# Kernel optimization log

Measured on AMD Instinct MI355X. Metric: run time of the kernel, lower is better.

## Reference

```python
import jax, jax.numpy as jnp
import numpy as np

NUM_USERS = 30000
NUM_ITEMS = 70000
N = NUM_USERS + NUM_ITEMS
D = 128
NNZ = 1_000_000
N_LAYERS = 3
BATCH = 16384
EPS = 1e-12  # torch F.normalize default eps
SLOPE = 0.01  # nn.LeakyReLU default negative_slope


def setup_inputs() -> dict:
    key = jax.random.key(0)
    ks = jax.random.split(key, 12)
    return {
        "userIdx": jax.random.randint(ks[0], (BATCH,), 0, NUM_USERS),
        "itemIdx": jax.random.randint(ks[1], (BATCH,), 0, NUM_ITEMS),
        "rows": jax.random.randint(ks[2], (NNZ,), 0, N),
        "cols": jax.random.randint(ks[3], (NNZ,), 0, N),
        "vals": jax.random.uniform(ks[4], (NNZ,), dtype=jnp.float32) * 0.1,
        "uEmbd": jax.random.normal(ks[5], (NUM_USERS, D), dtype=jnp.float32) * 0.1,
        "iEmbd": jax.random.normal(ks[6], (NUM_ITEMS, D), dtype=jnp.float32) * 0.1,
        "Wlin": jax.random.normal(ks[7], (N_LAYERS, D, D), dtype=jnp.float32) / np.sqrt(D),
        "blin": jax.random.normal(ks[8], (N_LAYERS, D), dtype=jnp.float32) * 0.01,
        "Wint": jax.random.normal(ks[9], (N_LAYERS, D, D), dtype=jnp.float32) / np.sqrt(D),
        "bint": jax.random.normal(ks[10], (N_LAYERS, D), dtype=jnp.float32) * 0.01,
    }


def reference(userIdx, itemIdx, rows, cols, vals, uEmbd, iEmbd, Wlin, blin, Wint, bint):
    num_users = uEmbd.shape[0]
    n = uEmbd.shape[0] + iEmbd.shape[0]
    features = jnp.concatenate([uEmbd, iEmbd], axis=0)  # [N, D]
    embds = [features]
    for l in range(Wlin.shape[0]):
        # SpMM: L @ features via gather + segment_sum over COO edges
        Lx = jax.ops.segment_sum(vals[:, None] * features[cols], rows, num_segments=n)
        # (L + I) @ f then linear
        part1 = (Lx + features) @ Wlin[l] + blin[l]
        # (L @ f) * f then linear
        part2 = (Lx * features) @ Wint[l] + bint[l]
        features = jax.nn.leaky_relu(part1 + part2, negative_slope=SLOPE)
        norm = jnp.maximum(jnp.linalg.norm(features, axis=1, keepdims=True), EPS)
        features = features / norm
        embds.append(features)
    finalEmbd = jnp.concatenate(embds, axis=1)  # [N, D*(1+n_layers)]
    u = finalEmbd[userIdx]
    i = finalEmbd[itemIdx + num_users]
    return jnp.sum(u * i, axis=1)
```

## Files before the change

kernel.cpp:

```cpp
#include <hip/hip_runtime.h>
#include <hip/hip_bf16.h>

#define NU 30000
#define NI 70000
#define NN 100000
#define DD 128
#define NLAYERS 3
#define SLOPE_ 0.01f
#define EPS_ 1e-12f

#define NB 782
#define NBKT 1024
#define NBLK 256
#define AROW 136
#define MAXL 32768
#define BM 64

typedef __bf16 v8bf __attribute__((ext_vector_type(8)));
typedef float v16f __attribute__((ext_vector_type(16)));
typedef float v2f __attribute__((ext_vector_type(2)));
typedef unsigned short ushort_t;

union UB8 { uint4 u; v8bf v; };

__device__ __forceinline__ float bflo(unsigned u) { return __uint_as_float(u << 16); }
__device__ __forceinline__ float bfhi(unsigned u) { return __uint_as_float(u & 0xffff0000u); }

__device__ __forceinline__ unsigned pk2(float a, float b) {
    __hip_bfloat162 h = __float22bfloat162_rn(make_float2(a, b));
    return *reinterpret_cast<unsigned*>(&h);
}
__device__ __forceinline__ uint4 pk8(const float* f) {
    return make_uint4(pk2(f[0], f[1]), pk2(f[2], f[3]), pk2(f[4], f[5]), pk2(f[6], f[7]));
}
__device__ __forceinline__ void unp8(uint4 g, float* f) {
    f[0] = bflo(g.x); f[1] = bfhi(g.x);
    f[2] = bflo(g.y); f[3] = bfhi(g.y);
    f[4] = bflo(g.z); f[5] = bfhi(g.z);
    f[6] = bflo(g.w); f[7] = bfhi(g.w);
}
__device__ __forceinline__ ushort_t f2bf1(float x) {
    __hip_bfloat16 h = __float2bfloat16(x);
    return *reinterpret_cast<ushort_t*>(&h);
}

__global__ __launch_bounds__(256) void k_concat_bf(const float* __restrict__ u,
                                                   const float* __restrict__ it,
                                                   ushort_t* __restrict__ fb) {
    int idx = blockIdx.x * 256 + threadIdx.x;
    if (idx >= NN * DD / 8) return;
    size_t base = (size_t)idx * 8;
    const float* src = (base < (size_t)NU * DD) ? (u + base) : (it + base - (size_t)NU * DD);
    float f[8];
    float4 a = *(const float4*)src;
    float4 b = *(const float4*)(src + 4);
    f[0] = a.x; f[1] = a.y; f[2] = a.z; f[3] = a.w;
    f[4] = b.x; f[5] = b.y; f[6] = b.z; f[7] = b.w;
    *(uint4*)(fb + base) = pk8(f);
}

__device__ __forceinline__ void dot_body(const ushort_t* __restrict__ fb,
                                         const int* __restrict__ uIdx,
                                         const int* __restrict__ iIdx,
                                         float* __restrict__ out,
                                         int batch, int accum, int blk, int t) {
    int b = blk * 4 + (t >> 6);
    if (b >= batch) return;
    int lane = t & 63;
    unsigned ua = *(const unsigned*)(fb + (size_t)uIdx[b] * DD + lane * 2);
    unsigned ib = *(const unsigned*)(fb + (size_t)(iIdx[b] + NU) * DD + lane * 2);
    float s = bflo(ua) * bflo(ib) + bfhi(ua) * bfhi(ib);
#pragma unroll
    for (int m = 32; m; m >>= 1) s += __shfl_xor(s, m, 64);
    if (lane == 0) out[b] = accum ? out[b] + s : s;
}

__global__ __launch_bounds__(256) void k_dot(const ushort_t* __restrict__ fb,
                                             const int* __restrict__ uIdx,
                                             const int* __restrict__ iIdx,
                                             float* __restrict__ out,
                                             int batch, int accum) {
    dot_body(fb, uIdx, iIdx, out, batch, accum, blockIdx.x, threadIdx.x);
}

__global__ __launch_bounds__(256) void k_lhist(const int* __restrict__ rows,
                                               int* __restrict__ ghist,
                                               int* __restrict__ flags,
                                               int nnz, int epb) {
    __shared__ int h[NBKT];
    int t = threadIdx.x, b = blockIdx.x;
#pragma unroll
    for (int i = 0; i < 4; ++i) h[t + 256 * i] = 0;
    for (int i = b * 256 + t; i < NN; i += NBLK * 256) flags[i] = 0;
    __syncthreads();
    int e0 = b * epb, e1 = min(e0 + epb, nnz);
    for (int e = e0 + t; e < e1; e += 256) atomicAdd(&h[rows[e] >> 7], 1);
    __syncthreads();
#pragma unroll
    for (int i = 0; i < 4; ++i) {
        int bkt = t + 256 * i;
        ghist[bkt * NBLK + b] = h[bkt];
    }
}

__global__ __launch_bounds__(256) void k_rscan(int* __restrict__ ghist,
                                               int* __restrict__ btot,
                                               const int* __restrict__ uIdx,
                                               const int* __restrict__ iIdx,
                                               int* __restrict__ flags,
                                               int* __restrict__ cnt, int batch) {
    int t = threadIdx.x;
    int gid = blockIdx.x * 256 + t;
    if (gid == 0) *cnt = 0;
    if (gid < batch) flags[uIdx[gid]] = 1;
    else if (gid < 2 * batch) flags[iIdx[gid - batch] + NU] = 1;

    int bkt = blockIdx.x * 4 + (t >> 6);
    int lane = t & 63;
    int* row = ghist + bkt * NBLK;
    int4 c = *(const int4*)(row + lane * 4);
    int s = c.x + c.y + c.z + c.w;
    int incl = s;
#pragma unroll
    for (int m = 1; m < 64; m <<= 1) {
        int o = __shfl_up(incl, m, 64);
        if (lane >= m) incl += o;
    }
    int excl = incl - s;
    int4 o;
    o.x = excl;
    o.y = o.x + c.x;
    o.z = o.y + c.y;
    o.w = o.z + c.z;
    *(int4*)(row + lane * 4) = o;
    if (lane == 63) btot[bkt] = incl;
}

__global__ __launch_bounds__(256) void k_btscan(const int* __restrict__ btot,
                                                int* __restrict__ bbase) {
    int t = threadIdx.x;
    int4 c = *(const int4*)(btot + t * 4);
    int tsum = c.x + c.y + c.z + c.w;
    int incl = tsum;
#pragma unroll
    for (int m = 1; m < 64; m <<= 1) {
        int o = __shfl_up(incl, m, 64);
        if ((t & 63) >= m) incl += o;
    }
    __shared__ int wsum[4];
    if ((t & 63) == 63) wsum[t >> 6] = incl;
    __syncthreads();
    int off = 0;
    for (int i = 0; i < (t >> 6); ++i) off += wsum[i];
    int excl = off + incl - tsum;
    int4 o;
    o.x = excl;
    o.y = o.x + c.x;
    o.z = o.y + c.y;
    o.w = o.z + c.z;
    *(int4*)(bbase + t * 4) = o;
    if (t == 255) bbase[NBKT] = o.w + c.w;
}

__global__ __launch_bounds__(256) void k_sscatter(const int* __restrict__ rows,
                                                  const int* __restrict__ cols,
                                                  const float* __restrict__ vals,
                                                  const int* __restrict__ ghist,
                                                  const int* __restrict__ bbase,
                                                  int2* __restrict__ bedges,
                                                  const int* __restrict__ flags,
                                                  int* __restrict__ list,
                                                  int* __restrict__ cnt,
                                                  int nnz, int epb) {
    __shared__ int base[NBKT];
    __shared__ int h[NBKT];
    int t = threadIdx.x, b = blockIdx.x;
#pragma unroll
    for (int i = 0; i < 4; ++i) {
        int bkt = t + 256 * i;
        base[bkt] = bbase[bkt] + ghist[bkt * NBLK + b];
        h[bkt] = 0;
    }
    int lane = t & 63;
    for (int i = b * 256 + t; i < ((NN + 65535) & ~65535); i += NBLK * 256) {
        int f = (i < NN) ? flags[i] : 0;
        unsigned long long mask = __ballot(f);
        int total = __popcll(mask);
        int prefix = __popcll(mask & ((1ULL << lane) - 1));
        int bs = 0;
        if (lane == 0 && total) bs = atomicAdd(cnt, total);
        bs = __shfl(bs, 0, 64);
        if (f) list[bs + prefix] = i;
    }
    __syncthreads();
    int e0 = b * epb, e1 = min(e0 + epb, nnz);
    for (int e = e0 + t; e < e1; e += 256) {
        int r = rows[e];
        int bkt = r >> 7;
        int rank = atomicAdd(&h[bkt], 1);
        bedges[base[bkt] + rank] = make_int2(((r & 127) << 20) | cols[e],
                                             __float_as_int(vals[e]));
    }
}

__global__ __launch_bounds__(256) void k_csort(const int* __restrict__ bbase,
                                               const int2* __restrict__ bedges,
                                               int2* __restrict__ edges,
                                               int* __restrict__ rowPtr, int nnz) {
    __shared__ int cntS[128];
    __shared__ int fillS[128];
    __shared__ int wtot;
    int b = blockIdx.x, t = threadIdx.x;
    int s0 = bbase[b];
    int s1 = bbase[b + 1];
    if (t < 128) cntS[t] = 0;
    __syncthreads();
    for (int i = s0 + t; i < s1; i += 256) atomicAdd(&cntS[bedges[i].x >> 20], 1);
    __syncthreads();
    int v = 0, incl = 0;
    if (t < 128) {
        v = cntS[t];
        incl = v;
#pragma unroll
        for (int m = 1; m < 64; m <<= 1) {
            int o = __shfl_up(incl, m, 64);
            if ((t & 63) >= m) incl += o;
        }
        if (t == 63) wtot = incl;
    }
    __syncthreads();
    if (t < 128) {
        int excl = incl - v + ((t >= 64) ? wtot : 0);
        fillS[t] = excl;
        int gr = b * 128 + t;
        if (gr < NN) rowPtr[gr] = s0 + excl;
    }
    if (b == 0 && t == 0) rowPtr[NN] = nnz;
    __syncthreads();
    for (int i = s0 + t; i < s1; i += 256) {
        int2 e = bedges[i];
        int r = e.x >> 20;
        int p = atomicAdd(&fillS[r], 1);
        edges[s0 + p] = make_int2(e.x & 0xFFFFF, e.y);
    }
}

__global__ __launch_bounds__(256) void k_wprep(const float* __restrict__ Wlin,
                                               const float* __restrict__ Wint,
                                               uint4* __restrict__ Wb4) {
    int id = blockIdx.x * 256 + threadIdx.x;
    int lane = id & 63;
    int w = (id >> 6) & 3;
    int s = (id >> 8) & 7;
    int c = (id >> 11) & 1;
    int l = id >> 12;
    const float* src = (c ? Wint : Wlin) + (size_t)l * DD * DD;
    int n = w * 32 + (lane & 31);
    int k0 = s * 16 + ((lane >> 5) & 1) * 8;
    float f[8];
#pragma unroll
    for (int j = 0; j < 8; ++j) f[j] = src[(size_t)(k0 + j) * DD + n];
    Wb4[id] = pk8(f);
}

__device__ __forceinline__ void acc_pk(v2f* acc2, uint4 g, float v) {
    v2f vv = {v, v};
    unsigned gw[4] = {g.x, g.y, g.z, g.w};
#pragma unroll
    for (int p = 0; p < 4; ++p) {
        v2f x = {bflo(gw[p]), bfhi(gw[p])};
        acc2[p] = x * vv + acc2[p];
    }
}

__device__ __forceinline__ void spmm_row(int r, int l,
                                         const int* __restrict__ rowPtr,
                                         const int2* __restrict__ edges,
                                         const ushort_t* __restrict__ fb,
                                         ushort_t* __restrict__ Lxb) {
    int q = l >> 4;
    int d0 = (l & 15) * 8;
    int beg = rowPtr[r], end = rowPtr[r + 1];
    v2f acc2[4];
#pragma unroll
    for (int p = 0; p < 4; ++p) acc2[p] = (v2f){0.f, 0.f};
    int e = beg + q;
    for (; e + 4 < end; e += 8) {
        int2 p0 = edges[e];
        int2 p1 = edges[e + 4];
        uint4 g0 = *(const uint4*)(fb + (size_t)p0.x * DD + d0);
        uint4 g1 = *(const uint4*)(fb + (size_t)p1.x * DD + d0);
        acc_pk(acc2, g0, __int_as_float(p0.y));
        acc_pk(acc2, g1, __int_as_float(p1.y));
    }
    if (e < end) {
        int2 p0 = edges[e];
        uint4 g0 = *(const uint4*)(fb + (size_t)p0.x * DD + d0);
        acc_pk(acc2, g0, __int_as_float(p0.y));
    }
    float acc[8];
#pragma unroll
    for (int p = 0; p < 4; ++p) { acc[2 * p] = acc2[p][0]; acc[2 * p + 1] = acc2[p][1]; }
#pragma unroll
    for (int j = 0; j < 8; ++j) {
        acc[j] += __shfl_xor(acc[j], 16, 64);
        acc[j] += __shfl_xor(acc[j], 32, 64);
    }
    if (l < 16) *(uint4*)(Lxb + (size_t)r * DD + d0) = pk8(acc);
}

__global__ __launch_bounds__(256) void k_spmm_dot(const int* __restrict__ rowPtr,
                                                  const int2* __restrict__ edges,
                                                  const ushort_t* __restrict__ fb,
                                                  ushort_t* __restrict__ Lxb,
                                                  const int* __restrict__ uIdx,
                                                  const int* __restrict__ iIdx,
                                                  float* __restrict__ out,
                                                  int batch, int accum, int dotBlocks) {
    if ((int)blockIdx.x < dotBlocks) {
        dot_body(fb, uIdx, iIdx, out, batch, accum, blockIdx.x, threadIdx.x);
        return;
    }
    int r = (blockIdx.x - dotBlocks) * 4 + (threadIdx.x >> 6);
    if (r >= NN) return;
    spmm_row(r, threadIdx.x & 63, rowPtr, edges, fb, Lxb);
}

__global__ __launch_bounds__(256) void k_spmm_idx_dot(const int* __restrict__ rowPtr,
                                                      const int2* __restrict__ edges,
                                                      const ushort_t* __restrict__ fb,
                                                      ushort_t* __restrict__ Lxb,
                                                      const int* __restrict__ list,
                                                      const int* __restrict__ cnt,
                                                      const int* __restrict__ uIdx,
                                                      const int* __restrict__ iIdx,
                                                      float* __restrict__ out,
                                                      int batch, int dotBlocks) {
    if ((int)blockIdx.x < dotBlocks) {
        dot_body(fb, uIdx, iIdx, out, batch, 1, blockIdx.x, threadIdx.x);
        return;
    }
    int i = (blockIdx.x - dotBlocks) * 4 + (threadIdx.x >> 6);
    if (i >= *cnt) return;
    spmm_row(list[i], threadIdx.x & 63, rowPtr, edges, fb, Lxb);
}

template <bool INDEXED>
__device__ __forceinline__ void layer_body(const ushort_t* __restrict__ Lxb,
                                           const uint4* __restrict__ Wb4,
                                           const float* __restrict__ blin,
                                           const float* __restrict__ bint,
                                           ushort_t* __restrict__ fb,
                                           const ushort_t* __restrict__ fin,
                                           const int* __restrict__ list, int nc) {
    __shared__ ushort_t As[BM * AROW];
    __shared__ float pnormAll[BM * 4];
    __shared__ float rinvS[BM];
    __shared__ int rowIdS[BM];

    const int t = threadIdx.x;
    const int w = t >> 6;
    const int l = t & 63;
    const int q = l >> 5;
    const int ln = l & 31;
    const int n = w * 32 + ln;
    const int m0 = blockIdx.x * BM;

    if (INDEXED && m0 >= nc) return;

    if (t < BM) {
        int gi = m0 + t;
        int gm;
        if (INDEXED) gm = (gi < nc) ? list[gi] : -1;
        else gm = (gi < NN) ? gi : -1;
        rowIdS[t] = gm;
    }
    __syncthreads();

    const float bias = blin[n] + bint[n];

    v16f acc[2];
#pragma unroll
    for (int mt = 0; mt < 2; ++mt)
#pragma unroll
        for (int i = 0; i < 16; ++i) acc[mt][i] = 0.f;

    for (int c = 0; c < 2; ++c) {
#pragma unroll
        for (int ii = 0; ii < 4; ++ii) {
            int idx = ii * 256 + t;
            int row = idx >> 4;
            int ch = idx & 15;
            int gm = rowIdS[row];
            uint4 outv = make_uint4(0, 0, 0, 0);
            if (gm >= 0) {
                uint4 gl = *(const uint4*)(Lxb + (size_t)gm * DD + ch * 8);
                uint4 gf = *(const uint4*)(fin + (size_t)gm * DD + ch * 8);
                float a[8], b[8], r[8];
                unp8(gl, a);
                unp8(gf, b);
                if (c == 0) {
#pragma unroll
                    for (int j = 0; j < 8; ++j) r[j] = a[j] + b[j];
                } else {
#pragma unroll
                    for (int j = 0; j < 8; ++j) r[j] = a[j] * b[j];
                }
                outv = pk8(r);
            }
            *(uint4*)&As[row * AROW + ch * 8] = outv;
        }
        __syncthreads();

        UB8 bf[8];
#pragma unroll
        for (int s = 0; s < 8; ++s) bf[s].u = Wb4[c * 2048 + s * 256 + w * 64 + l];

#pragma unroll
        for (int mt = 0; mt < 2; ++mt) {
#pragma unroll
            for (int s = 0; s < 8; ++s) {
                v8bf af = *(const v8bf*)&As[(mt * 32 + ln) * AROW + s * 16 + q * 8];
                acc[mt] = __builtin_amdgcn_mfma_f32_32x32x16_bf16(af, bf[s].v, acc[mt], 0, 0, 0);
            }
        }
        __syncthreads();
    }

#pragma unroll
    for (int mt = 0; mt < 2; ++mt) {
        float r[16];
#pragma unroll
        for (int reg = 0; reg < 16; ++reg) {
            float v = acc[mt][reg] + bias;
            v = (v > 0.f) ? v : SLOPE_ * v;
            acc[mt][reg] = v;
            r[reg] = v * v;
        }
#pragma unroll
        for (int lev = 0; lev < 4; ++lev) {
            int m = 1 << lev;
            int cnt2 = 8 >> lev;
            bool hi = (l & m) != 0;
#pragma unroll
            for (int i = 0; i < 8; ++i) {
                if (i < cnt2) {
                    float p = hi ? r[2 * i + 1] : r[2 * i];
                    float qv = hi ? r[2 * i] : r[2 * i + 1];
                    r[i] = p + __shfl_xor(qv, m, 64);
                }
            }
        }
        float tot = r[0] + __shfl_xor(r[0], 16, 64);
        if ((l & 31) < 16) {
            int i = l & 15;
            int row = (i & 3) + ((i >> 2) << 3) + 4 * q;
            pnormAll[(mt * 32 + row) * 4 + w] = tot;
        }
    }
    __syncthreads();
    if (t < BM) {
        float4 p = *(const float4*)&pnormAll[t * 4];
        float tot = p.x + p.y + p.z + p.w;
        rinvS[t] = 1.0f / fmaxf(sqrtf(tot), EPS_);
    }
    __syncthreads();

#pragma unroll
    for (int mt = 0; mt < 2; ++mt) {
#pragma unroll
        for (int reg = 0; reg < 16; ++reg) {
            int row = (reg & 3) + ((reg >> 2) << 3) + 4 * q;
            int gm = rowIdS[mt * 32 + row];
            if (gm >= 0)
                fb[(size_t)gm * DD + n] = f2bf1(acc[mt][reg] * rinvS[mt * 32 + row]);
        }
    }
}

__global__ __launch_bounds__(256, 4) void k_layer2(const ushort_t* __restrict__ Lxb,
                                                   const uint4* __restrict__ Wb4,
                                                   const float* __restrict__ blin,
                                                   const float* __restrict__ bint,
                                                   const ushort_t* __restrict__ fin,
                                                   ushort_t* __restrict__ fb) {
    layer_body<false>(Lxb, Wb4, blin, bint, fb, fin, nullptr, 0);
}

__global__ __launch_bounds__(256, 4) void k_layer_idx(const ushort_t* __restrict__ Lxb,
                                                      const uint4* __restrict__ Wb4,
                                                      const float* __restrict__ blin,
                                                      const float* __restrict__ bint,
                                                      const ushort_t* __restrict__ fin,
                                                      ushort_t* __restrict__ fb,
                                                      const int* __restrict__ list,
                                                      const int* __restrict__ cnt) {
    layer_body<true>(Lxb, Wb4, blin, bint, fb, fin, list, *cnt);
}

extern "C" void kernel_launch(void* const* d_in, const int* in_sizes, int n_in,
                              void* d_out, int out_size, void* d_ws, size_t ws_size,
                              hipStream_t stream) {
    const int*   userIdx = (const int*)d_in[0];
    const int*   itemIdx = (const int*)d_in[1];
    const int*   rows    = (const int*)d_in[2];
    const int*   cols    = (const int*)d_in[3];
    const float* vals    = (const float*)d_in[4];
    const float* uE      = (const float*)d_in[5];
    const float* iE      = (const float*)d_in[6];
    const float* Wlin    = (const float*)d_in[7];
    const float* blin    = (const float*)d_in[8];
    const float* Wint    = (const float*)d_in[9];
    const float* bint    = (const float*)d_in[10];
    float* out = (float*)d_out;

    const int batch = in_sizes[0];
    const int nnz   = in_sizes[2];
    const int epb   = (nnz + NBLK - 1) / NBLK;
    const int dotBlocks = (batch + 3) / 4;

    ushort_t* featA = (ushort_t*)d_ws;
    ushort_t* featB = featA + (size_t)NN * DD;
    ushort_t* Lxb   = featB + (size_t)NN * DD;
    uint4* Wb4      = (uint4*)(Lxb + (size_t)NN * DD);
    int2*  bedges   = (int2*)(Wb4 + 12288);
    int2*  edges    = bedges + nnz;
    int*   ghist    = (int*)(edges + nnz);
    int*   btot     = ghist + NBKT * NBLK;
    int*   bbase    = btot + NBKT;
    int*   rowPtr   = bbase + NBKT + 4;
    int*   flags    = rowPtr + NN + 4;
    int*   list     = flags + NN;
    int*   cnt      = list + MAXL;

    k_concat_bf<<<(NN * DD / 8 + 255) / 256, 256, 0, stream>>>(uE, iE, featA);
    k_wprep<<<48, 256, 0, stream>>>(Wlin, Wint, Wb4);

    k_lhist<<<NBLK, 256, 0, stream>>>(rows, ghist, flags, nnz, epb);
    k_rscan<<<NBKT / 4, 256, 0, stream>>>(ghist, btot, userIdx, itemIdx, flags, cnt, batch);
    k_btscan<<<1, 256, 0, stream>>>(btot, bbase);
    k_sscatter<<<NBLK, 256, 0, stream>>>(rows, cols, vals, ghist, bbase, bedges,
                                         flags, list, cnt, nnz, epb);
    k_csort<<<NB, 256, 0, stream>>>(bbase, bedges, edges, rowPtr, nnz);

    k_spmm_dot<<<dotBlocks + (NN + 3) / 4, 256, 0, stream>>>(
        rowPtr, edges, featA, Lxb, userIdx, itemIdx, out, batch, 0, dotBlocks);
    k_layer2<<<(NN + BM - 1) / BM, 256, 0, stream>>>(
        Lxb, Wb4, blin, bint, featA, featB);

    k_spmm_dot<<<dotBlocks + (NN + 3) / 4, 256, 0, stream>>>(
        rowPtr, edges, featB, Lxb, userIdx, itemIdx, out, batch, 1, dotBlocks);
    k_layer2<<<(NN + BM - 1) / BM, 256, 0, stream>>>(
        Lxb, Wb4 + 4096, blin + DD, bint + DD, featB, featA);

    k_spmm_idx_dot<<<dotBlocks + (MAXL + 3) / 4, 256, 0, stream>>>(
        rowPtr, edges, featA, Lxb, list, cnt, userIdx, itemIdx, out, batch, dotBlocks);
    k_layer_idx<<<(MAXL + BM - 1) / BM, 256, 0, stream>>>(
        Lxb, Wb4 + 8192, blin + 2 * DD, bint + 2 * DD, featA, featB, list, cnt);

    k_dot<<<dotBlocks, 256, 0, stream>>>(featB, userIdx, itemIdx, out, batch, 1);
}
```

Measured before the change: 366.6 us.

## Merge prep kernels and precompute Lx+f and Lx*f in SpMM epilogue

Three setup kernels (bf16 concat, weight repack, row histogram) are merged into one launch dispatched by block index, which removes two launch gaps. The SpMM epilogue now reads the row's own features and writes both (Lx+f) and (Lx*f) as bf16 into a doubled-width buffer. The layer GEMM then loads its A operand directly instead of re-reading Lx and f and combining them. This doubles the bytes written by SpMM, but drops one input stream and the elementwise work from the layer kernel.

```diff
diff --git a/kernel.cpp b/kernel.cpp
--- a/kernel.cpp
+++ b/kernel.cpp
@@ -16,6 +16,9 @@
 #define MAXL 32768
 #define BM 64
 
+#define CONCAT_B 6250
+#define WPREP_B 48
+
 typedef __bf16 v8bf __attribute__((ext_vector_type(8)));
 typedef float v16f __attribute__((ext_vector_type(16)));
 typedef float v2f __attribute__((ext_vector_type(2)));
@@ -42,21 +45,6 @@
 __device__ __forceinline__ ushort_t f2bf1(float x) {
     __hip_bfloat16 h = __float2bfloat16(x);
     return *reinterpret_cast<ushort_t*>(&h);
-}
-
-__global__ __launch_bounds__(256) void k_concat_bf(const float* __restrict__ u,
-                                                   const float* __restrict__ it,
-                                                   ushort_t* __restrict__ fb) {
-    int idx = blockIdx.x * 256 + threadIdx.x;
-    if (idx >= NN * DD / 8) return;
-    size_t base = (size_t)idx * 8;
-    const float* src = (base < (size_t)NU * DD) ? (u + base) : (it + base - (size_t)NU * DD);
-    float f[8];
-    float4 a = *(const float4*)src;
-    float4 b = *(const float4*)(src + 4);
-    f[0] = a.x; f[1] = a.y; f[2] = a.z; f[3] = a.w;
-    f[4] = b.x; f[5] = b.y; f[6] = b.z; f[7] = b.w;
-    *(uint4*)(fb + base) = pk8(f);
 }
 
 __device__ __forceinline__ void dot_body(const ushort_t* __restrict__ fb,
@@ -83,12 +71,50 @@
     dot_body(fb, uIdx, iIdx, out, batch, accum, blockIdx.x, threadIdx.x);
 }
 
-__global__ __launch_bounds__(256) void k_lhist(const int* __restrict__ rows,
-                                               int* __restrict__ ghist,
-                                               int* __restrict__ flags,
-                                               int nnz, int epb) {
+__global__ __launch_bounds__(256) void k_prep(const float* __restrict__ uE,
+                                              const float* __restrict__ iE,
+                                              ushort_t* __restrict__ featA,
+                                              const float* __restrict__ Wlin,
+                                              const float* __restrict__ Wint,
+                                              uint4* __restrict__ Wb4,
+                                              const int* __restrict__ rows,
+                                              int* __restrict__ ghist,
+                                              int* __restrict__ flags,
+                                              int nnz, int epb) {
     __shared__ int h[NBKT];
-    int t = threadIdx.x, b = blockIdx.x;
+    int t = threadIdx.x;
+    int blk = blockIdx.x;
+
+    if (blk < CONCAT_B) {
+        int idx = blk * 256 + t;
+        if (idx >= NN * DD / 8) return;
+        size_t base = (size_t)idx * 8;
+        const float* src = (base < (size_t)NU * DD) ? (uE + base) : (iE + base - (size_t)NU * DD);
+        float f[8];
+        float4 a = *(const float4*)src;
+        float4 b4 = *(const float4*)(src + 4);
+        f[0] = a.x; f[1] = a.y; f[2] = a.z; f[3] = a.w;
+        f[4] = b4.x; f[5] = b4.y; f[6] = b4.z; f[7] = b4.w;
+        *(uint4*)(featA + base) = pk8(f);
+        return;
+    }
+    if (blk < CONCAT_B + WPREP_B) {
+        int id = (blk - CONCAT_B) * 256 + t;
+        int lane = id & 63;
+        int w = (id >> 6) & 3;
+        int s = (id >> 8) & 7;
+        int c = (id >> 11) & 1;
+        int l = id >> 12;
+        const float* src = (c ? Wint : Wlin) + (size_t)l * DD * DD;
+        int n = w * 32 + (lane & 31);
+        int k0 = s * 16 + ((lane >> 5) & 1) * 8;
+        float f[8];
+#pragma unroll
+        for (int j = 0; j < 8; ++j) f[j] = src[(size_t)(k0 + j) * DD + n];
+        Wb4[id] = pk8(f);
+        return;
+    }
+    int b = blk - CONCAT_B - WPREP_B;
 #pragma unroll
     for (int i = 0; i < 4; ++i) h[t + 256 * i] = 0;
     for (int i = b * 256 + t; i < NN; i += NBLK * 256) flags[i] = 0;
@@ -245,24 +271,6 @@
     }
 }
 
-__global__ __launch_bounds__(256) void k_wprep(const float* __restrict__ Wlin,
-                                               const float* __restrict__ Wint,
-                                               uint4* __restrict__ Wb4) {
-    int id = blockIdx.x * 256 + threadIdx.x;
-    int lane = id & 63;
-    int w = (id >> 6) & 3;
-    int s = (id >> 8) & 7;
-    int c = (id >> 11) & 1;
-    int l = id >> 12;
-    const float* src = (c ? Wint : Wlin) + (size_t)l * DD * DD;
-    int n = w * 32 + (lane & 31);
-    int k0 = s * 16 + ((lane >> 5) & 1) * 8;
-    float f[8];
-#pragma unroll
-    for (int j = 0; j < 8; ++j) f[j] = src[(size_t)(k0 + j) * DD + n];
-    Wb4[id] = pk8(f);
-}
-
 __device__ __forceinline__ void acc_pk(v2f* acc2, uint4 g, float v) {
     v2f vv = {v, v};
     unsigned gw[4] = {g.x, g.y, g.z, g.w};
@@ -277,7 +285,7 @@
                                          const int* __restrict__ rowPtr,
                                          const int2* __restrict__ edges,
                                          const ushort_t* __restrict__ fb,
-                                         ushort_t* __restrict__ Lxb) {
+                                         ushort_t* __restrict__ AM) {
     int q = l >> 4;
     int d0 = (l & 15) * 8;
     int beg = rowPtr[r], end = rowPtr[r + 1];
@@ -306,13 +314,22 @@
         acc[j] += __shfl_xor(acc[j], 16, 64);
         acc[j] += __shfl_xor(acc[j], 32, 64);
     }
-    if (l < 16) *(uint4*)(Lxb + (size_t)r * DD + d0) = pk8(acc);
+    if (l < 16) {
+        uint4 gf = *(const uint4*)(fb + (size_t)r * DD + d0);
+        float f8[8];
+        unp8(gf, f8);
+        float ad[8], ml[8];
+#pragma unroll
+        for (int j = 0; j < 8; ++j) { ad[j] = acc[j] + f8[j]; ml[j] = acc[j] * f8[j]; }
+        *(uint4*)(AM + (size_t)r * 256 + d0) = pk8(ad);
+        *(uint4*)(AM + (size_t)r * 256 + 128 + d0) = pk8(ml);
+    }
 }
 
 __global__ __launch_bounds__(256) void k_spmm_dot(const int* __restrict__ rowPtr,
                                                   const int2* __restrict__ edges,
                                                   const ushort_t* __restrict__ fb,
-                                                  ushort_t* __restrict__ Lxb,
+                                                  ushort_t* __restrict__ AM,
                                                   const int* __restrict__ uIdx,
                                                   const int* __restrict__ iIdx,
                                                   float* __restrict__ out,
@@ -323,13 +340,13 @@
     }
     int r = (blockIdx.x - dotBlocks) * 4 + (threadIdx.x >> 6);
     if (r >= NN) return;
-    spmm_row(r, threadIdx.x & 63, rowPtr, edges, fb, Lxb);
+    spmm_row(r, threadIdx.x & 63, rowPtr, edges, fb, AM);
 }
 
 __global__ __launch_bounds__(256) void k_spmm_idx_dot(const int* __restrict__ rowPtr,
                                                       const int2* __restrict__ edges,
                                                       const ushort_t* __restrict__ fb,
-                                                      ushort_t* __restrict__ Lxb,
+                                                      ushort_t* __restrict__ AM,
                                                       const int* __restrict__ list,
                                                       const int* __restrict__ cnt,
                                                       const int* __restrict__ uIdx,
@@ -342,16 +359,15 @@
     }
     int i = (blockIdx.x - dotBlocks) * 4 + (threadIdx.x >> 6);
     if (i >= *cnt) return;
-    spmm_row(list[i], threadIdx.x & 63, rowPtr, edges, fb, Lxb);
+    spmm_row(list[i], threadIdx.x & 63, rowPtr, edges, fb, AM);
 }
 
 template <bool INDEXED>
-__device__ __forceinline__ void layer_body(const ushort_t* __restrict__ Lxb,
+__device__ __forceinline__ void layer_body(const ushort_t* __restrict__ AM,
                                            const uint4* __restrict__ Wb4,
                                            const float* __restrict__ blin,
                                            const float* __restrict__ bint,
                                            ushort_t* __restrict__ fb,
-                                           const ushort_t* __restrict__ fin,
                                            const int* __restrict__ list, int nc) {
     __shared__ ushort_t As[BM * AROW];
     __shared__ float pnormAll[BM * 4];
@@ -392,23 +408,10 @@
             int row = idx >> 4;
             int ch = idx & 15;
             int gm = rowIdS[row];
-            uint4 outv = make_uint4(0, 0, 0, 0);
-            if (gm >= 0) {
-                uint4 gl = *(const uint4*)(Lxb + (size_t)gm * DD + ch * 8);
-                uint4 gf = *(const uint4*)(fin + (size_t)gm * DD + ch * 8);
-                float a[8], b[8], r[8];
-                unp8(gl, a);
-                unp8(gf, b);
-                if (c == 0) {
-#pragma unroll
-                    for (int j = 0; j < 8; ++j) r[j] = a[j] + b[j];
-                } else {
-#pragma unroll
-                    for (int j = 0; j < 8; ++j) r[j] = a[j] * b[j];
-                }
-                outv = pk8(r);
-            }
-            *(uint4*)&As[row * AROW + ch * 8] = outv;
+            uint4 v = make_uint4(0, 0, 0, 0);
+            if (gm >= 0)
+                v = *(const uint4*)(AM + (size_t)gm * 256 + c * 128 + ch * 8);
+            *(uint4*)&As[row * AROW + ch * 8] = v;
         }
         __syncthreads();
 
@@ -478,24 +481,22 @@
     }
 }
 
-__global__ __launch_bounds__(256, 4) void k_layer2(const ushort_t* __restrict__ Lxb,
+__global__ __launch_bounds__(256, 4) void k_layer2(const ushort_t* __restrict__ AM,
                                                    const uint4* __restrict__ Wb4,
                                                    const float* __restrict__ blin,
                                                    const float* __restrict__ bint,
-                                                   const ushort_t* __restrict__ fin,
                                                    ushort_t* __restrict__ fb) {
-    layer_body<false>(Lxb, Wb4, blin, bint, fb, fin, nullptr, 0);
-}
-
-__global__ __launch_bounds__(256, 4) void k_layer_idx(const ushort_t* __restrict__ Lxb,
+    layer_body<false>(AM, Wb4, blin, bint, fb, nullptr, 0);
+}
+
+__global__ __launch_bounds__(256, 4) void k_layer_idx(const ushort_t* __restrict__ AM,
                                                       const uint4* __restrict__ Wb4,
                                                       const float* __restrict__ blin,
                                                       const float* __restrict__ bint,
-                                                      const ushort_t* __restrict__ fin,
                                                       ushort_t* __restrict__ fb,
                                                       const int* __restrict__ list,
                                                       const int* __restrict__ cnt) {
-    layer_body<true>(Lxb, Wb4, blin, bint, fb, fin, list, *cnt);
+    layer_body<true>(AM, Wb4, blin, bint, fb, list, *cnt);
 }
 
 extern "C" void kernel_launch(void* const* d_in, const int* in_sizes, int n_in,
@@ -521,8 +522,8 @@
 
     ushort_t* featA = (ushort_t*)d_ws;
     ushort_t* featB = featA + (size_t)NN * DD;
-    ushort_t* Lxb   = featB + (size_t)NN * DD;
-    uint4* Wb4      = (uint4*)(Lxb + (size_t)NN * DD);
+    ushort_t* AM    = featB + (size_t)NN * DD;
+    uint4* Wb4      = (uint4*)(AM + (size_t)NN * 256);
     int2*  bedges   = (int2*)(Wb4 + 12288);
     int2*  edges    = bedges + nnz;
     int*   ghist    = (int*)(edges + nnz);
@@ -533,10 +534,9 @@
     int*   list     = flags + NN;
     int*   cnt      = list + MAXL;
 
-    k_concat_bf<<<(NN * DD / 8 + 255) / 256, 256, 0, stream>>>(uE, iE, featA);
-    k_wprep<<<48, 256, 0, stream>>>(Wlin, Wint, Wb4);
-
-    k_lhist<<<NBLK, 256, 0, stream>>>(rows, ghist, flags, nnz, epb);
+    k_prep<<<CONCAT_B + WPREP_B + NBLK, 256, 0, stream>>>(
+        uE, iE, featA, Wlin, Wint, Wb4, rows, ghist, flags, nnz, epb);
+
     k_rscan<<<NBKT / 4, 256, 0, stream>>>(ghist, btot, userIdx, itemIdx, flags, cnt, batch);
     k_btscan<<<1, 256, 0, stream>>>(btot, bbase);
     k_sscatter<<<NBLK, 256, 0, stream>>>(rows, cols, vals, ghist, bbase, bedges,
@@ -544,19 +544,18 @@
     k_csort<<<NB, 256, 0, stream>>>(bbase, bedges, edges, rowPtr, nnz);
 
     k_spmm_dot<<<dotBlocks + (NN + 3) / 4, 256, 0, stream>>>(
-        rowPtr, edges, featA, Lxb, userIdx, itemIdx, out, batch, 0, dotBlocks);
+        rowPtr, edges, featA, AM, userIdx, itemIdx, out, batch, 0, dotBlocks);
+    k_layer2<<<(NN + BM - 1) / BM, 256, 0, stream>>>(AM, Wb4, blin, bint, featB);
+
+    k_spmm_dot<<<dotBlocks + (NN + 3) / 4, 256, 0, stream>>>(
+        rowPtr, edges, featB, AM, userIdx, itemIdx, out, batch, 1, dotBlocks);
     k_layer2<<<(NN + BM - 1) / BM, 256, 0, stream>>>(
-        Lxb, Wb4, blin, bint, featA, featB);
-
-    k_spmm_dot<<<dotBlocks + (NN + 3) / 4, 256, 0, stream>>>(
-        rowPtr, edges, featB, Lxb, userIdx, itemIdx, out, batch, 1, dotBlocks);
-    k_layer2<<<(NN + BM - 1) / BM, 256, 0, stream>>>(
-        Lxb, Wb4 + 4096, blin + DD, bint + DD, featB, featA);
+        AM, Wb4 + 4096, blin + DD, bint + DD, featA);
 
     k_spmm_idx_dot<<<dotBlocks + (MAXL + 3) / 4, 256, 0, stream>>>(
-        rowPtr, edges, featA, Lxb, list, cnt, userIdx, itemIdx, out, batch, dotBlocks);
+        rowPtr, edges, featA, AM, list, cnt, userIdx, itemIdx, out, batch, dotBlocks);
     k_layer_idx<<<(MAXL + BM - 1) / BM, 256, 0, stream>>>(
-        Lxb, Wb4 + 8192, blin + 2 * DD, bint + 2 * DD, featA, featB, list, cnt);
+        AM, Wb4 + 8192, blin + 2 * DD, bint + 2 * DD, featB, list, cnt);
 
     k_dot<<<dotBlocks, 256, 0, stream>>>(featB, userIdx, itemIdx, out, batch, 1);
 }
```

New measurement: 372.2 us. About the same (+1.5%).
